# Optimization experiments

Hardware: AMD Instinct MI355X
Metric: run time of the kernel (lower is better)

Reference implementation:

```python
import jax, jax.numpy as jnp
import numpy as np

B, N, D = 4, 1024, 2048
H_Q, H_KV = 16, 4
D_HEAD = D // H_Q            # 128
GROUPS = H_Q // H_KV         # 4
ROPE_BASE = 10000.0


def rms_norm(x, w, eps):
    # normalize over last dim (d_head), learnable scale w
    ms = jnp.mean(jnp.square(x), axis=-1, keepdims=True)
    return x * jax.lax.rsqrt(ms + eps) * w


def apply_rope(t, pos):
    # t: (B, H, N, d). Half-split RoPE rotation.
    d = t.shape[-1]
    inv_freq = 1.0 / (ROPE_BASE ** (jnp.arange(0, d, 2, dtype=jnp.float32) / d))  # (d/2,)
    ang = pos.astype(jnp.float32)[:, None] * inv_freq[None, :]                     # (N, d/2)
    cos, sin = jnp.cos(ang), jnp.sin(ang)                                          # (N, d/2)
    t1, t2 = t[..., : d // 2], t[..., d // 2 :]
    return jnp.concatenate([t1 * cos - t2 * sin, t2 * cos + t1 * sin], axis=-1)


def setup_inputs() -> dict:
    key = jax.random.key(0)
    ks = jax.random.split(key, 4)
    x = jax.random.normal(ks[0], (B, N, D), dtype=jnp.float32)
    w_qkv = jax.random.normal(ks[1], (D_HEAD * (H_Q + 2 * H_KV), D), dtype=jnp.float32) * (D ** -0.5)
    w_out = jax.random.normal(ks[2], (D, D), dtype=jnp.float32) * (D ** -0.5)
    q_norm_w = jnp.ones((D_HEAD,), dtype=jnp.float32)
    k_norm_w = jnp.ones((D_HEAD,), dtype=jnp.float32)
    mask = jnp.triu(jnp.ones((N, N), dtype=bool), k=1)  # True = masked (causal)
    pos = jnp.arange(N, dtype=jnp.int64) if jax.config.jax_enable_x64 else jnp.arange(N, dtype=jnp.int32)
    return {"x": x, "mask": mask, "pos": pos, "w_qkv": w_qkv, "w_out": w_out,
            "q_norm_w": q_norm_w, "k_norm_w": k_norm_w}


def reference(x, mask, pos, w_qkv, w_out, q_norm_w, k_norm_w):
    eps = jnp.finfo(x.dtype).eps
    scale = D_HEAD ** -0.5
    # fused QKV projection, split into heads
    qkv = jnp.einsum('bnd,ed->bne', x, w_qkv)                       # (B, N, (Hq+2Hkv)*d)
    qkv = qkv.reshape(B, N, H_Q + 2 * H_KV, D_HEAD).transpose(0, 2, 1, 3)
    q, k, v = jnp.split(qkv, [H_Q, H_Q + H_KV], axis=1)             # (B,Hq,N,d),(B,Hkv,N,d)x2
    # qk RMSNorm
    q = rms_norm(q, q_norm_w, eps)
    k = rms_norm(k, k_norm_w, eps)
    # RoPE
    q = apply_rope(q, pos)
    k = apply_rope(k, pos)
    # GQA: repeat kv heads across groups
    k = jnp.repeat(k, GROUPS, axis=1)                               # (B, Hq, N, d)
    v = jnp.repeat(v, GROUPS, axis=1)
    # manual attention (non-flash path)
    scores = jnp.einsum('bhqd,bhkd->bhqk', q, k) * scale            # (B, Hq, N, N)
    scores = jnp.where(mask, -jnp.inf, scores)
    attn = jax.nn.softmax(scores, axis=-1)
    y = jnp.einsum('bhqk,bhkd->bhqd', attn, v)                      # (B, Hq, N, d)
    y = y.transpose(0, 2, 1, 3).reshape(B, N, D)
    return jnp.einsum('bnd,ed->bne', y, w_out)                      # out_proj
```

## Files before the change

### kernel.cpp

```cpp
#include <hip/hip_runtime.h>
#include <cstdint>
#include <cstddef>

#define B_   4
#define N_   1024
#define D_   2048
#define HQ_  16
#define HKV_ 4
#define DH_  128
#define E_   3072

#define SCALE_ 0.08838834764831845

typedef __attribute__((ext_vector_type(8))) short frag16;
typedef __attribute__((ext_vector_type(4))) float fragf4;
#define MFMA16(a, b, c) __builtin_amdgcn_mfma_f32_16x16x32_bf16(a, b, c, 0, 0, 0)

__device__ __forceinline__ short f2bf(float f) {
  union { float f; uint32_t u; } a; a.f = f;
  uint32_t r = (a.u + 0x7fffu + ((a.u >> 16) & 1u)) >> 16;
  return (short)r;
}
__device__ __forceinline__ short f2bf_t(float f) {
  union { float f; uint32_t u; } a; a.f = f;
  return (short)(a.u >> 16);
}
__device__ __forceinline__ void async_copy16(const void* g, void* l) {
  __builtin_amdgcn_global_load_lds(
      (const __attribute__((address_space(1))) void*)g,
      (__attribute__((address_space(3))) void*)l, 16, 0, 0);
}

__global__ __launch_bounds__(256) void f2bf_kernel(const float* __restrict__ src,
                                                   short* __restrict__ dst, int n) {
  const int i = (blockIdx.x * 256 + threadIdx.x) * 8;
  if (i >= n) return;
  float4 a = *(const float4*)(src + i);
  float4 b = *(const float4*)(src + i + 4);
  union { frag16 f; short s[8]; } u;
  u.s[0] = f2bf(a.x); u.s[1] = f2bf(a.y); u.s[2] = f2bf(a.z); u.s[3] = f2bf(a.w);
  u.s[4] = f2bf(b.x); u.s[5] = f2bf(b.y); u.s[6] = f2bf(b.z); u.s[7] = f2bf(b.w);
  *(frag16*)(dst + i) = u.f;
}

template <typename OutT>
__global__ __launch_bounds__(256) void gemm_mfma(const short* __restrict__ A,
                                                 const short* __restrict__ Wt,
                                                 OutT* __restrict__ C,
                                                 int Nc, int K, int ncpx) {
  __shared__ __align__(16) short As[128][32];
  __shared__ __align__(16) short Bs[128][32];

  const int bid = blockIdx.x;
  const int xcd = bid & 7, j = bid >> 3;
  const int m0 = (j & 31) * 128;
  const int n0 = (xcd * ncpx + (j >> 5)) * 128;

  const int tid = threadIdx.x;
  const int lane = tid & 63;
  const int w = tid >> 6;
  const int ln = lane & 15, g = lane >> 4;
  const int wm = (w >> 1) * 64, wn = (w & 1) * 64;

  const int srow = lane >> 2;
  const int scol = (((lane & 3) - ((lane >> 3) & 3)) & 3) * 8;
  const int rcol = ((g + (ln >> 1)) & 3) * 8;

  fragf4 acc[4][4];
#pragma unroll
  for (int i = 0; i < 4; ++i)
#pragma unroll
    for (int jj = 0; jj < 4; ++jj) acc[i][jj] = (fragf4){0.f, 0.f, 0.f, 0.f};

  for (int k0 = 0; k0 < K; k0 += 32) {
    __syncthreads();
#pragma unroll
    for (int i = 0; i < 2; ++i) {
      const int slab = w * 2 + i;
      const int r = slab * 16 + srow;
      async_copy16(A  + (size_t)(m0 + r) * K + k0 + scol, &As[slab * 16][0]);
      async_copy16(Wt + (size_t)(n0 + r) * K + k0 + scol, &Bs[slab * 16][0]);
    }
    __syncthreads();

    frag16 af[4], bf[4];
#pragma unroll
    for (int t = 0; t < 4; ++t) {
      af[t] = *(const frag16*)&As[wm + t * 16 + ln][rcol];
      bf[t] = *(const frag16*)&Bs[wn + t * 16 + ln][rcol];
    }
#pragma unroll
    for (int i = 0; i < 4; ++i)
#pragma unroll
      for (int jj = 0; jj < 4; ++jj) acc[i][jj] = MFMA16(af[i], bf[jj], acc[i][jj]);
  }

#pragma unroll
  for (int i = 0; i < 4; ++i) {
#pragma unroll
    for (int jj = 0; jj < 4; ++jj) {
#pragma unroll
      for (int r = 0; r < 4; ++r) {
        const size_t idx = (size_t)(m0 + wm + i * 16 + 4 * g + r) * Nc +
                           (n0 + wn + jj * 16 + ln);
        if constexpr (sizeof(OutT) == 2) C[idx] = f2bf(acc[i][jj][r]);
        else                             C[idx] = acc[i][jj][r];
      }
    }
  }
}

__global__ __launch_bounds__(256) void normrope(short* __restrict__ qkvb,
                                                const int* __restrict__ pos,
                                                const float* __restrict__ qw,
                                                const float* __restrict__ kw) {
  const int gid = blockIdx.x * 256 + threadIdx.x;
  const int lane = gid & 63;
  const int wid = gid >> 6;
  const int hh = wid % (HQ_ + HKV_);
  const int n  = (wid / (HQ_ + HKV_)) % N_;
  const int b  = wid / ((HQ_ + HKV_) * N_);

  int eoff; const float* w;
  if (hh < HQ_) { eoff = hh * DH_;              w = qw; }
  else          { eoff = D_ + (hh - HQ_) * DH_; w = kw; }

  short* base = qkvb + ((size_t)b * N_ + n) * E_ + eoff;
  union { uint32_t u; float f; } c1, c2;
  c1.u = ((uint32_t)(uint16_t)base[lane]) << 16;
  c2.u = ((uint32_t)(uint16_t)base[64 + lane]) << 16;
  float t1 = c1.f, t2 = c2.f;

  float ss = t1 * t1 + t2 * t2;
#pragma unroll
  for (int off = 32; off; off >>= 1) ss += __shfl_xor(ss, off);
  const float r = rsqrtf(ss * (1.0f / 128.0f) + 1.1920928955078125e-07f);
  t1 = t1 * r * w[lane];
  t2 = t2 * r * w[64 + lane];

  const float invf = (float)exp2(-(double)lane * 0.20762050593046014);
  const float ang = (float)pos[n] * invf;
  const float c = cosf(ang), s = sinf(ang);
  base[lane]      = f2bf(t1 * c - t2 * s);
  base[64 + lane] = f2bf(t2 * c + t1 * s);
}

__global__ __launch_bounds__(256) void vtrans(const short* __restrict__ qkvb,
                                              short* __restrict__ vtg) {
  __shared__ short T[128 * 72];
  const int n0 = blockIdx.x * 64, kh = blockIdx.y, b = blockIdx.z;
  const int tid = threadIdx.x;
  {
    const int r = tid & 63, dc = (tid >> 6) * 32;
    const short* src = qkvb + ((size_t)b * N_ + n0 + r) * E_ + 2560 + kh * DH_ + dc;
    union { frag16 f; short s[8]; } u;
#pragma unroll
    for (int i = 0; i < 4; ++i) {
      u.f = *(const frag16*)(src + 8 * i);
#pragma unroll
      for (int jj = 0; jj < 8; ++jj) T[(dc + 8 * i + jj) * 72 + r] = u.s[jj];
    }
  }
  __syncthreads();
  {
    const int d = tid & 127, e = tid >> 7;
    short* dst = vtg + ((size_t)(b * HKV_ + kh) * DH_ + d) * N_ + n0 + e * 32;
#pragma unroll
    for (int i = 0; i < 4; ++i)
      *(frag16*)(dst + 8 * i) = *(const frag16*)&T[d * 72 + e * 32 + 8 * i];
  }
}

__global__ __launch_bounds__(256) void attn_mfma(const short* __restrict__ qkvb,
                                                 const short* __restrict__ vtg,
                                                 short* __restrict__ yb) {
  const int bx = blockIdx.x;
  const int qt = 63 - (bx >> 4);
  const int id = bx & 15;
  const int kh = id & 3, b = id >> 2;
  const int q0 = qt * 16;

  __shared__ __align__(16) short lds_[22600];
  const int VT0 = 8704, PS0 = 17992;

  const int tid = threadIdx.x;
  const int lane = tid & 63;
  const int w = tid >> 6;
  const int ln = lane & 15, g = lane >> 4, g8 = g * 8;
  const int h = kh * 4 + w;

  const short* qb = qkvb + (size_t)b * N_ * E_ + h * DH_;
  const short* kb = qkvb + (size_t)b * N_ * E_ + D_ + kh * DH_;
  const short* vt = vtg + (size_t)(b * HKV_ + kh) * DH_ * N_;

  if (tid < 64) lds_[VT0 + 128 * 72 + tid] = (short)0x3F80;

  frag16 qf[4];
  {
    const short* qrow = qb + (size_t)(q0 + ln) * E_ + g8;
#pragma unroll
    for (int c = 0; c < 4; ++c) qf[c] = *(const frag16*)(qrow + c * 32);
  }

  fragf4 o[8], ol = (fragf4){0.f, 0.f, 0.f, 0.f};
#pragma unroll
  for (int dt = 0; dt < 8; ++dt) o[dt] = (fragf4){0.f, 0.f, 0.f, 0.f};

  const float SC2 = (float)(SCALE_ * 1.4426950408889634);
  const float MB2 = (float)(12.0 * 1.4426950408889634);

  const int ntiles = qt / 4 + 1;
  for (int kt = 0; kt < ntiles; ++kt) {
    const int kbase = kt * 64;
    __syncthreads();
    {
      const int r = tid & 63, c = (tid >> 6) * 32;
      const short* src = kb + (size_t)(kbase + r) * E_ + c;
#pragma unroll
      for (int i = 0; i < 4; ++i)
        *(frag16*)&lds_[r * 136 + c + 8 * i] = *(const frag16*)(src + 8 * i);
    }
    {
      const int d = tid & 127, e = tid >> 7;
      const short* src = vt + (size_t)d * N_ + kbase + e * 32;
#pragma unroll
      for (int i = 0; i < 4; ++i)
        *(frag16*)&lds_[VT0 + d * 72 + e * 32 + 8 * i] = *(const frag16*)(src + 8 * i);
    }
    __syncthreads();

    fragf4 s[4];
#pragma unroll
    for (int st = 0; st < 4; ++st) s[st] = (fragf4){0.f, 0.f, 0.f, 0.f};
#pragma unroll
    for (int c = 0; c < 4; ++c) {
      frag16 qc = qf[c];
#pragma unroll
      for (int st = 0; st < 4; ++st) {
        frag16 kf = *(const frag16*)&lds_[(st * 16 + ln) * 136 + c * 32 + g8];
        s[st] = MFMA16(qc, kf, s[st]);
      }
    }

    const bool full = (kbase + 63) <= q0;
#pragma unroll
    for (int st = 0; st < 4; ++st) {
      const int kg = kbase + st * 16 + ln;
#pragma unroll
      for (int r2 = 0; r2 < 4; ++r2) {
        float sv = s[st][r2];
        if (!full && kg > q0 + 4 * g + r2) sv = -1.0e30f;
        const float p = exp2f(fmaf(sv, SC2, -MB2));
        lds_[PS0 + (w * 16 + 4 * g + r2) * 72 + st * 16 + ln] = f2bf_t(p);
      }
    }

    frag16 pf0 = *(const frag16*)&lds_[PS0 + (w * 16 + ln) * 72 + g8];
    frag16 pf1 = *(const frag16*)&lds_[PS0 + (w * 16 + ln) * 72 + 32 + g8];
#pragma unroll
    for (int dt = 0; dt < 8; ++dt) {
      frag16 v0 = *(const frag16*)&lds_[VT0 + (dt * 16 + ln) * 72 + g8];
      frag16 v1 = *(const frag16*)&lds_[VT0 + (dt * 16 + ln) * 72 + 32 + g8];
      o[dt] = MFMA16(pf0, v0, o[dt]);
      o[dt] = MFMA16(pf1, v1, o[dt]);
    }
    {
      frag16 vl0 = *(const frag16*)&lds_[VT0 + (128 + ln) * 72 + g8];
      frag16 vl1 = *(const frag16*)&lds_[VT0 + (128 + ln) * 72 + 32 + g8];
      ol = MFMA16(pf0, vl0, ol);
      ol = MFMA16(pf1, vl1, ol);
    }
  }

#pragma unroll
  for (int r2 = 0; r2 < 4; ++r2) {
    const float lv = __shfl(ol[r2], lane & 48);
    const float inv = 1.0f / lv;
    short* yrow = yb + ((size_t)b * N_ + q0 + 4 * g + r2) * D_ + h * DH_;
#pragma unroll
    for (int dt = 0; dt < 8; ++dt) yrow[dt * 16 + ln] = f2bf(o[dt][r2] * inv);
  }
}

extern "C" void kernel_launch(void* const* d_in, const int* in_sizes, int n_in,
                              void* d_out, int out_size, void* d_ws, size_t ws_size,
                              hipStream_t stream) {
  const float* x     = (const float*)d_in[0];
  const int*   pos   = (const int*)d_in[2];
  const float* w_qkv = (const float*)d_in[3];
  const float* w_out = (const float*)d_in[4];
  const float* qw    = (const float*)d_in[5];
  const float* kw    = (const float*)d_in[6];
  float* out = (float*)d_out;

  short* qkvb = (short*)d_ws;
  short* yb   = qkvb + (size_t)B_ * N_ * E_;
  short* xb   = yb   + (size_t)B_ * N_ * D_;
  short* wqb  = xb   + (size_t)B_ * N_ * D_;
  short* wob  = wqb  + (size_t)E_ * D_;
  short* vtg  = xb;

  const int nx = B_ * N_ * D_, nwq = E_ * D_, nwo = D_ * D_;
  f2bf_kernel<<<nx  / 2048, 256, 0, stream>>>(x,     xb,  nx);
  f2bf_kernel<<<nwq / 2048, 256, 0, stream>>>(w_qkv, wqb, nwq);
  f2bf_kernel<<<nwo / 2048, 256, 0, stream>>>(w_out, wob, nwo);

  gemm_mfma<short><<<768, 256, 0, stream>>>(xb, wqb, qkvb, E_, D_, 3);

  normrope<<<(B_ * N_ * (HQ_ + HKV_) * 64) / 256, 256, 0, stream>>>(
      qkvb, pos, qw, kw);

  vtrans<<<dim3(N_ / 64, HKV_, B_), 256, 0, stream>>>(qkvb, vtg);

  attn_mfma<<<1024, 256, 0, stream>>>(qkvb, vtg, yb);

  gemm_mfma<float><<<512, 256, 0, stream>>>(yb, wob, out, D_, D_, 2);
}
```

Before: 328.0 us.

## Double GEMM K-tile with XOR swizzle and merge small elementwise launches

The GEMM K step grows from 32 to 64 with 128x64 LDS tiles and an XOR-swizzled chunk layout, which halves the number of barrier pairs per K and issues twice as many MFMAs per sync. The three fp32-to-bf16 conversion launches are merged into one grid. The normrope and V-transpose kernels become a single launch that branches on block index. Both merges cut launch overhead. Because normrope rewrites only the Q/K columns and the transpose reads only the V columns, the two branches have no data race.

```diff
diff --git a/kernel.cpp b/kernel.cpp
--- a/kernel.cpp
+++ b/kernel.cpp
@@ -31,16 +31,22 @@
       (__attribute__((address_space(3))) void*)l, 16, 0, 0);
 }
 
-__global__ __launch_bounds__(256) void f2bf_kernel(const float* __restrict__ src,
-                                                   short* __restrict__ dst, int n) {
-  const int i = (blockIdx.x * 256 + threadIdx.x) * 8;
-  if (i >= n) return;
-  float4 a = *(const float4*)(src + i);
-  float4 b = *(const float4*)(src + i + 4);
-  union { frag16 f; short s[8]; } u;
-  u.s[0] = f2bf(a.x); u.s[1] = f2bf(a.y); u.s[2] = f2bf(a.z); u.s[3] = f2bf(a.w);
-  u.s[4] = f2bf(b.x); u.s[5] = f2bf(b.y); u.s[6] = f2bf(b.z); u.s[7] = f2bf(b.w);
-  *(frag16*)(dst + i) = u.f;
+__global__ __launch_bounds__(256) void f2bf3_kernel(
+    const float* __restrict__ s0, short* __restrict__ d0, int b0,
+    const float* __restrict__ s1, short* __restrict__ d1, int b1,
+    const float* __restrict__ s2, short* __restrict__ d2) {
+  int bx = blockIdx.x;
+  const float* s; short* d;
+  if (bx < b0)           { s = s0; d = d0; }
+  else if (bx < b0 + b1) { s = s1; d = d1; bx -= b0; }
+  else                   { s = s2; d = d2; bx -= b0 + b1; }
+  const int i = (bx * 256 + threadIdx.x) * 8;
+  float4 a = *(const float4*)(s + i);
+  float4 b = *(const float4*)(s + i + 4);
+  union { frag16 f; short sh[8]; } u;
+  u.sh[0] = f2bf(a.x); u.sh[1] = f2bf(a.y); u.sh[2] = f2bf(a.z); u.sh[3] = f2bf(a.w);
+  u.sh[4] = f2bf(b.x); u.sh[5] = f2bf(b.y); u.sh[6] = f2bf(b.z); u.sh[7] = f2bf(b.w);
+  *(frag16*)(d + i) = u.f;
 }
 
 template <typename OutT>
@@ -48,8 +54,8 @@
                                                  const short* __restrict__ Wt,
                                                  OutT* __restrict__ C,
                                                  int Nc, int K, int ncpx) {
-  __shared__ __align__(16) short As[128][32];
-  __shared__ __align__(16) short Bs[128][32];
+  __shared__ __align__(16) short As[128][64];
+  __shared__ __align__(16) short Bs[128][64];
 
   const int bid = blockIdx.x;
   const int xcd = bid & 7, j = bid >> 3;
@@ -62,9 +68,9 @@
   const int ln = lane & 15, g = lane >> 4;
   const int wm = (w >> 1) * 64, wn = (w & 1) * 64;
 
-  const int srow = lane >> 2;
-  const int scol = (((lane & 3) - ((lane >> 3) & 3)) & 3) * 8;
-  const int rcol = ((g + (ln >> 1)) & 3) * 8;
+  const int srow = lane >> 3;
+  const int schunk = ((lane & 7) ^ srow) * 8;
+  const int l7 = ln & 7;
 
   fragf4 acc[4][4];
 #pragma unroll
@@ -72,27 +78,34 @@
 #pragma unroll
     for (int jj = 0; jj < 4; ++jj) acc[i][jj] = (fragf4){0.f, 0.f, 0.f, 0.f};
 
-  for (int k0 = 0; k0 < K; k0 += 32) {
-    __syncthreads();
-#pragma unroll
-    for (int i = 0; i < 2; ++i) {
-      const int slab = w * 2 + i;
-      const int r = slab * 16 + srow;
-      async_copy16(A  + (size_t)(m0 + r) * K + k0 + scol, &As[slab * 16][0]);
-      async_copy16(Wt + (size_t)(n0 + r) * K + k0 + scol, &Bs[slab * 16][0]);
-    }
-    __syncthreads();
-
-    frag16 af[4], bf[4];
-#pragma unroll
-    for (int t = 0; t < 4; ++t) {
-      af[t] = *(const frag16*)&As[wm + t * 16 + ln][rcol];
-      bf[t] = *(const frag16*)&Bs[wn + t * 16 + ln][rcol];
-    }
-#pragma unroll
-    for (int i = 0; i < 4; ++i)
-#pragma unroll
-      for (int jj = 0; jj < 4; ++jj) acc[i][jj] = MFMA16(af[i], bf[jj], acc[i][jj]);
+  for (int k0 = 0; k0 < K; k0 += 64) {
+    __syncthreads();
+#pragma unroll
+    for (int i = 0; i < 4; ++i) {
+      const int rbase = w * 32 + i * 8;
+      const int r = rbase + srow;
+      async_copy16(A  + (size_t)(m0 + r) * K + k0 + schunk, &As[rbase][0]);
+      async_copy16(Wt + (size_t)(n0 + r) * K + k0 + schunk, &Bs[rbase][0]);
+    }
+    __syncthreads();
+
+    frag16 af[2][4], bf[2][4];
+#pragma unroll
+    for (int c = 0; c < 2; ++c) {
+      const int pc = (((c << 2) | g) ^ l7) * 8;
+#pragma unroll
+      for (int t = 0; t < 4; ++t) {
+        af[c][t] = *(const frag16*)&As[wm + t * 16 + ln][pc];
+        bf[c][t] = *(const frag16*)&Bs[wn + t * 16 + ln][pc];
+      }
+    }
+#pragma unroll
+    for (int c = 0; c < 2; ++c)
+#pragma unroll
+      for (int i = 0; i < 4; ++i)
+#pragma unroll
+        for (int jj = 0; jj < 4; ++jj)
+          acc[i][jj] = MFMA16(af[c][i], bf[c][jj], acc[i][jj]);
   }
 
 #pragma unroll
@@ -110,64 +123,67 @@
   }
 }
 
-__global__ __launch_bounds__(256) void normrope(short* __restrict__ qkvb,
-                                                const int* __restrict__ pos,
-                                                const float* __restrict__ qw,
-                                                const float* __restrict__ kw) {
-  const int gid = blockIdx.x * 256 + threadIdx.x;
-  const int lane = gid & 63;
-  const int wid = gid >> 6;
-  const int hh = wid % (HQ_ + HKV_);
-  const int n  = (wid / (HQ_ + HKV_)) % N_;
-  const int b  = wid / ((HQ_ + HKV_) * N_);
-
-  int eoff; const float* w;
-  if (hh < HQ_) { eoff = hh * DH_;              w = qw; }
-  else          { eoff = D_ + (hh - HQ_) * DH_; w = kw; }
-
-  short* base = qkvb + ((size_t)b * N_ + n) * E_ + eoff;
-  union { uint32_t u; float f; } c1, c2;
-  c1.u = ((uint32_t)(uint16_t)base[lane]) << 16;
-  c2.u = ((uint32_t)(uint16_t)base[64 + lane]) << 16;
-  float t1 = c1.f, t2 = c2.f;
-
-  float ss = t1 * t1 + t2 * t2;
-#pragma unroll
-  for (int off = 32; off; off >>= 1) ss += __shfl_xor(ss, off);
-  const float r = rsqrtf(ss * (1.0f / 128.0f) + 1.1920928955078125e-07f);
-  t1 = t1 * r * w[lane];
-  t2 = t2 * r * w[64 + lane];
-
-  const float invf = (float)exp2(-(double)lane * 0.20762050593046014);
-  const float ang = (float)pos[n] * invf;
-  const float c = cosf(ang), s = sinf(ang);
-  base[lane]      = f2bf(t1 * c - t2 * s);
-  base[64 + lane] = f2bf(t2 * c + t1 * s);
-}
-
-__global__ __launch_bounds__(256) void vtrans(const short* __restrict__ qkvb,
-                                              short* __restrict__ vtg) {
+__global__ __launch_bounds__(256) void normrope_vt(short* __restrict__ qkvb,
+                                                   short* __restrict__ vtg,
+                                                   const int* __restrict__ pos,
+                                                   const float* __restrict__ qw,
+                                                   const float* __restrict__ kw,
+                                                   int nrB) {
   __shared__ short T[128 * 72];
-  const int n0 = blockIdx.x * 64, kh = blockIdx.y, b = blockIdx.z;
   const int tid = threadIdx.x;
-  {
-    const int r = tid & 63, dc = (tid >> 6) * 32;
-    const short* src = qkvb + ((size_t)b * N_ + n0 + r) * E_ + 2560 + kh * DH_ + dc;
-    union { frag16 f; short s[8]; } u;
-#pragma unroll
-    for (int i = 0; i < 4; ++i) {
-      u.f = *(const frag16*)(src + 8 * i);
-#pragma unroll
-      for (int jj = 0; jj < 8; ++jj) T[(dc + 8 * i + jj) * 72 + r] = u.s[jj];
-    }
-  }
-  __syncthreads();
-  {
-    const int d = tid & 127, e = tid >> 7;
-    short* dst = vtg + ((size_t)(b * HKV_ + kh) * DH_ + d) * N_ + n0 + e * 32;
-#pragma unroll
-    for (int i = 0; i < 4; ++i)
-      *(frag16*)(dst + 8 * i) = *(const frag16*)&T[d * 72 + e * 32 + 8 * i];
+
+  if ((int)blockIdx.x < nrB) {
+    const int gid = blockIdx.x * 256 + tid;
+    const int lane = gid & 63;
+    const int wid = gid >> 6;
+    const int hh = wid % (HQ_ + HKV_);
+    const int n  = (wid / (HQ_ + HKV_)) % N_;
+    const int b  = wid / ((HQ_ + HKV_) * N_);
+
+    int eoff; const float* w;
+    if (hh < HQ_) { eoff = hh * DH_;              w = qw; }
+    else          { eoff = D_ + (hh - HQ_) * DH_; w = kw; }
+
+    short* base = qkvb + ((size_t)b * N_ + n) * E_ + eoff;
+    union { uint32_t u; float f; } c1, c2;
+    c1.u = ((uint32_t)(uint16_t)base[lane]) << 16;
+    c2.u = ((uint32_t)(uint16_t)base[64 + lane]) << 16;
+    float t1 = c1.f, t2 = c2.f;
+
+    float ss = t1 * t1 + t2 * t2;
+#pragma unroll
+    for (int off = 32; off; off >>= 1) ss += __shfl_xor(ss, off);
+    const float r = rsqrtf(ss * (1.0f / 128.0f) + 1.1920928955078125e-07f);
+    t1 = t1 * r * w[lane];
+    t2 = t2 * r * w[64 + lane];
+
+    const float invf = (float)exp2(-(double)lane * 0.20762050593046014);
+    const float ang = (float)pos[n] * invf;
+    const float c = cosf(ang), s = sinf(ang);
+    base[lane]      = f2bf(t1 * c - t2 * s);
+    base[64 + lane] = f2bf(t2 * c + t1 * s);
+  } else {
+    const int idx = blockIdx.x - nrB;
+    const int n0 = (idx & 15) * 64, kh = (idx >> 4) & 3, b = idx >> 6;
+    {
+      const int r = tid & 63, dc = (tid >> 6) * 32;
+      const short* src = qkvb + ((size_t)b * N_ + n0 + r) * E_ + 2560 + kh * DH_ + dc;
+      union { frag16 f; short s[8]; } u;
+#pragma unroll
+      for (int i = 0; i < 4; ++i) {
+        u.f = *(const frag16*)(src + 8 * i);
+#pragma unroll
+        for (int jj = 0; jj < 8; ++jj) T[(dc + 8 * i + jj) * 72 + r] = u.s[jj];
+      }
+    }
+    __syncthreads();
+    {
+      const int d = tid & 127, e = tid >> 7;
+      short* dst = vtg + ((size_t)(b * HKV_ + kh) * DH_ + d) * N_ + n0 + e * 32;
+#pragma unroll
+      for (int i = 0; i < 4; ++i)
+        *(frag16*)(dst + 8 * i) = *(const frag16*)&T[d * 72 + e * 32 + 8 * i];
+    }
   }
 }
 
@@ -301,16 +317,14 @@
   short* vtg  = xb;
 
   const int nx = B_ * N_ * D_, nwq = E_ * D_, nwo = D_ * D_;
-  f2bf_kernel<<<nx  / 2048, 256, 0, stream>>>(x,     xb,  nx);
-  f2bf_kernel<<<nwq / 2048, 256, 0, stream>>>(w_qkv, wqb, nwq);
-  f2bf_kernel<<<nwo / 2048, 256, 0, stream>>>(w_out, wob, nwo);
+  const int bx_ = nx / 2048, bwq = nwq / 2048, bwo = nwo / 2048;
+  f2bf3_kernel<<<bx_ + bwq + bwo, 256, 0, stream>>>(
+      x, xb, bx_, w_qkv, wqb, bwq, w_out, wob);
 
   gemm_mfma<short><<<768, 256, 0, stream>>>(xb, wqb, qkvb, E_, D_, 3);
 
-  normrope<<<(B_ * N_ * (HQ_ + HKV_) * 64) / 256, 256, 0, stream>>>(
-      qkvb, pos, qw, kw);
-
-  vtrans<<<dim3(N_ / 64, HKV_, B_), 256, 0, stream>>>(qkvb, vtg);
+  const int nrB = (B_ * N_ * (HQ_ + HKV_) * 64) / 256;
+  normrope_vt<<<nrB + 256, 256, 0, stream>>>(qkvb, vtg, pos, qw, kw, nrB);
 
   attn_mfma<<<1024, 256, 0, stream>>>(qkvb, vtg, yb);
 
```

After: 304.1 us. -7.3%, faster.
